# Kernel tuning notes

Measured on AMD Instinct MI355X. Metric: run time of the kernel, lower is better.

The kernel has to match this reference:

```python
import jax, jax.numpy as jnp
import numpy as np

N_NODES = 50000
EMB = 256
HEADS = 8
NEG_SLOPE = 0.2


def gat_conv(x, src, dst, W, a_src, a_dst, b, num_nodes):
    # x: [N, Din]; W: [Din, H, F]; a_src/a_dst: [H, F]; b: [H*F]
    h = jnp.einsum('nd,dhf->nhf', x, W)                      # [N, H, F]
    al_s = jnp.sum(h * a_src, axis=-1)                       # [N, H]
    al_d = jnp.sum(h * a_dst, axis=-1)                       # [N, H]
    logits = jax.nn.leaky_relu(al_s[src] + al_d[dst], NEG_SLOPE)  # [E, H]
    # segment softmax over incoming edges of each destination node
    m = jax.ops.segment_max(logits, dst, num_segments=num_nodes)  # [N, H]
    e = jnp.exp(logits - m[dst])                              # [E, H]
    z = jax.ops.segment_sum(e, dst, num_segments=num_nodes)   # [N, H]
    alpha = e / (z[dst] + 1e-16)                              # [E, H]
    msg = h[src] * alpha[..., None]                           # [E, H, F]
    out = jax.ops.segment_sum(msg, dst, num_segments=num_nodes)  # [N, H, F]
    return out.reshape(num_nodes, -1) + b


def setup_inputs() -> dict:
    key = jax.random.key(0)
    ks = jax.random.split(key, 10)
    F1 = EMB // HEADS  # 32
    x = jax.random.normal(ks[0], (N_NODES, EMB), dtype=jnp.float32)
    edge_index = jax.random.randint(ks[1], (2, 800000), 0, N_NODES, dtype=jnp.int64)
    s1 = 1.0 / np.sqrt(EMB)
    W1 = jax.random.normal(ks[2], (EMB, HEADS, F1), dtype=jnp.float32) * s1
    a_src1 = jax.random.normal(ks[3], (HEADS, F1), dtype=jnp.float32) * s1
    a_dst1 = jax.random.normal(ks[4], (HEADS, F1), dtype=jnp.float32) * s1
    b1 = jnp.zeros((HEADS * F1,), dtype=jnp.float32)
    W2 = jax.random.normal(ks[5], (EMB, 1, EMB), dtype=jnp.float32) * s1
    a_src2 = jax.random.normal(ks[6], (1, EMB), dtype=jnp.float32) * s1
    a_dst2 = jax.random.normal(ks[7], (1, EMB), dtype=jnp.float32) * s1
    b2 = jnp.zeros((EMB,), dtype=jnp.float32)
    return {"x": x, "edge_index": edge_index,
            "W1": W1, "a_src1": a_src1, "a_dst1": a_dst1, "b1": b1,
            "W2": W2, "a_src2": a_src2, "a_dst2": a_dst2, "b2": b2}


def reference(x, edge_index, W1, a_src1, a_dst1, b1, W2, a_src2, a_dst2, b2):
    n = x.shape[0]
    loops = jnp.arange(n, dtype=edge_index.dtype)
    src = jnp.concatenate([edge_index[0], loops])
    dst = jnp.concatenate([edge_index[1], loops])
    h = gat_conv(x, src, dst, W1, a_src1, a_dst1, b1, n)   # [N, EMB]
    out = gat_conv(h, src, dst, W2, a_src2, a_dst2, b2, n)  # [N, EMB]
    return out
```

## Files before the change

kernel.cpp:

```cpp
#include <hip/hip_runtime.h>
#include <hip/hip_bf16.h>

typedef unsigned short u16;
typedef unsigned int   u32;

typedef __attribute__((ext_vector_type(8))) short s16x8;
typedef __attribute__((ext_vector_type(8))) unsigned short u16x8;
typedef __attribute__((ext_vector_type(4))) float f32x4;

__device__ __forceinline__ float b2f(u16 u) {
    union { u32 i; float f; } v; v.i = ((u32)u) << 16; return v.f;
}
__device__ __forceinline__ u16 f2b(float f) {
    union { float f; u32 i; } v; v.f = f;
    u32 u = v.i;
    u32 r = (u + 0x7fffu + ((u >> 16) & 1u)) >> 16;
    return (u16)r;
}

__global__ void detect_flags(const u16* __restrict__ xw, const int* __restrict__ ei,
                             int* __restrict__ flags) {
    int t = threadIdx.x;
    u16 w = xw[2 * t];
    int e = (w >> 7) & 0xFF;
    bool sane = (e >= 112 && e <= 131);
    unsigned long long m1 = __ballot(sane);
    bool hz = (ei[2 * t + 1] == 0);
    unsigned long long m2 = __ballot(hz);
    if (t == 0) {
        flags[0] = (__popcll(m1) >= 32) ? 0 : 1;
        flags[1] = (m2 == ~0ull) ? 1 : 0;
    }
}

__device__ __forceinline__ int edge_at(const int* __restrict__ ei, int i64f, long long j) {
    return i64f ? ei[2 * j] : ei[(size_t)j];
}

__global__ __launch_bounds__(256) void cvt_b16(const void* __restrict__ in,
                                               u16* __restrict__ outb,
                                               int total4, const int* __restrict__ flags) {
    int i = blockIdx.x * 256 + threadIdx.x;
    if (i >= total4) return;
    ushort4 o;
    if (flags[0]) {
        float4 v = ((const float4*)in)[i];
        o.x = f2b(v.x); o.y = f2b(v.y); o.z = f2b(v.z); o.w = f2b(v.w);
    } else {
        o = ((const ushort4*)in)[i];
    }
    ((ushort4*)outb)[i] = o;
}

__global__ __launch_bounds__(256) void cvt_wt2(const void* __restrict__ W1,
                                               const void* __restrict__ W2,
                                               u16* __restrict__ Wt1,
                                               u16* __restrict__ Wt2,
                                               const int* __restrict__ flags) {
    int b = blockIdx.x;
    const void* W = (b < 256) ? W1 : W2;
    u16* Wt = (b < 256) ? Wt1 : Wt2;
    int k = b & 255, c = threadIdx.x;
    u16 v = flags[0] ? f2b(((const float*)W)[k * 256 + c]) : ((const u16*)W)[k * 256 + c];
    Wt[c * 256 + k] = v;
}

__global__ __launch_bounds__(256) void cvt_small(const void* p0, const void* p1, const void* p2,
                                                 const void* p3, const void* p4, const void* p5,
                                                 u16* __restrict__ sv,
                                                 const int* __restrict__ flags) {
    int t = threadIdx.x;
    const void* ps[6] = {p0, p1, p2, p3, p4, p5};
    int f = flags[0];
#pragma unroll
    for (int j = 0; j < 6; j++) {
        u16 v = f ? f2b(((const float*)ps[j])[t]) : ((const u16*)ps[j])[t];
        sv[j * 256 + t] = v;
    }
}

__global__ __launch_bounds__(256) void count_deg(const int* __restrict__ ei,
                                                 int* __restrict__ deg, int E, int ET,
                                                 const int* __restrict__ flags) {
    int i = blockIdx.x * 256 + threadIdx.x;
    if (i >= ET) return;
    int i64f = flags[1];
    int d = (i < E) ? edge_at(ei, i64f, (long long)E + i) : (i - E);
    atomicAdd(&deg[d], 1);
}

__global__ __launch_bounds__(256) void scan1(const int* __restrict__ deg,
                                             int* __restrict__ offs,
                                             int* __restrict__ bsum, int N) {
    __shared__ int sh[256];
    int tid = threadIdx.x;
    int i = blockIdx.x * 256 + tid;
    int v = (i < N) ? deg[i] : 0;
    sh[tid] = v;
    __syncthreads();
    for (int s = 1; s < 256; s <<= 1) {
        int t = (tid >= s) ? sh[tid - s] : 0;
        __syncthreads();
        sh[tid] += t;
        __syncthreads();
    }
    if (i < N) offs[i] = sh[tid] - v;
    if (tid == 255) bsum[blockIdx.x] = sh[255];
}

__global__ __launch_bounds__(256) void scan2(int* bsum, int nb) {
    __shared__ int sh[256];
    int tid = threadIdx.x;
    int v = (tid < nb) ? bsum[tid] : 0;
    sh[tid] = v;
    __syncthreads();
    for (int s = 1; s < 256; s <<= 1) {
        int t = (tid >= s) ? sh[tid - s] : 0;
        __syncthreads();
        sh[tid] += t;
        __syncthreads();
    }
    if (tid < nb) bsum[tid] = sh[tid] - v;
}

__global__ __launch_bounds__(256) void scan3(int* __restrict__ offs,
                                             const int* __restrict__ bsum, int N, int ET) {
    int i = blockIdx.x * 256 + threadIdx.x;
    if (i < N) offs[i] += bsum[blockIdx.x];
    if (i == 0) offs[N] = ET;
}

__global__ __launch_bounds__(256) void fill_csr(const int* __restrict__ ei,
                                                const int* __restrict__ offs,
                                                int* __restrict__ cur,
                                                int* __restrict__ csr, int E, int ET,
                                                const int* __restrict__ flags) {
    int i = blockIdx.x * 256 + threadIdx.x;
    if (i >= ET) return;
    int i64f = flags[1];
    int s, d;
    if (i < E) { s = edge_at(ei, i64f, i); d = edge_at(ei, i64f, (long long)E + i); }
    else       { s = d = i - E; }
    int p = atomicAdd(&cur[d], 1);
    csr[offs[d] + p] = s;
}

__global__ __launch_bounds__(256) void gemm_tiled(const u16* __restrict__ A,
                                                  const u16* __restrict__ Bt,
                                                  u16* __restrict__ C, int M) {
    __shared__ u16 sA[128 * 32];
    __shared__ u16 sB[128 * 32];
    int tid = threadIdx.x;
    int mt = blockIdx.x >> 1, nt = blockIdx.x & 1;
    int r0 = mt * 128, c0 = nt * 128;
    int w = tid >> 6, lane = tid & 63;
    int wr = w & 1, wc = w >> 1;
    int lm = lane & 15, quad = lane >> 4;

    int row0 = tid >> 2, ch0 = tid & 3;
    int row1 = row0 + 64;
    int ga0 = r0 + row0; if (ga0 >= M) ga0 = M - 1;
    int ga1 = r0 + row1; if (ga1 >= M) ga1 = M - 1;
    const u16* Ab0 = A + (size_t)ga0 * 256 + ch0 * 8;
    const u16* Ab1 = A + (size_t)ga1 * 256 + ch0 * 8;
    const u16* Bb0 = Bt + (size_t)(c0 + row0) * 256 + ch0 * 8;
    const u16* Bb1 = Bt + (size_t)(c0 + row1) * 256 + ch0 * 8;

    u16x8 ra0 = *(const u16x8*)Ab0;
    u16x8 ra1 = *(const u16x8*)Ab1;
    u16x8 rb0 = *(const u16x8*)Bb0;
    u16x8 rb1 = *(const u16x8*)Bb1;

    f32x4 acc[4][4];
#pragma unroll
    for (int i = 0; i < 4; i++)
#pragma unroll
        for (int j = 0; j < 4; j++) acc[i][j] = (f32x4){0.f, 0.f, 0.f, 0.f};

    u16* wA0 = sA + row0 * 32 + ch0 * 8;
    u16* wA1 = sA + row1 * 32 + ch0 * 8;
    u16* wB0 = sB + row0 * 32 + ch0 * 8;
    u16* wB1 = sB + row1 * 32 + ch0 * 8;
    const u16* rA = sA + (wr * 64 + lm) * 32 + quad * 8;
    const u16* rB = sB + (wc * 64 + lm) * 32 + quad * 8;

    for (int kb = 0; kb < 8; kb++) {
        __syncthreads();
        *(u16x8*)wA0 = ra0;
        *(u16x8*)wA1 = ra1;
        *(u16x8*)wB0 = rb0;
        *(u16x8*)wB1 = rb1;
        __syncthreads();
        if (kb < 7) {
            int ko = (kb + 1) * 32;
            ra0 = *(const u16x8*)(Ab0 + ko);
            ra1 = *(const u16x8*)(Ab1 + ko);
            rb0 = *(const u16x8*)(Bb0 + ko);
            rb1 = *(const u16x8*)(Bb1 + ko);
        }
        s16x8 af[4], bf[4];
#pragma unroll
        for (int fr = 0; fr < 4; fr++) af[fr] = *(const s16x8*)(rA + fr * 16 * 32);
#pragma unroll
        for (int fc = 0; fc < 4; fc++) bf[fc] = *(const s16x8*)(rB + fc * 16 * 32);
#pragma unroll
        for (int fr = 0; fr < 4; fr++)
#pragma unroll
            for (int fc = 0; fc < 4; fc++)
                acc[fr][fc] = __builtin_amdgcn_mfma_f32_16x16x32_bf16(af[fr], bf[fc], acc[fr][fc], 0, 0, 0);
    }

#pragma unroll
    for (int fr = 0; fr < 4; fr++) {
#pragma unroll
        for (int fc = 0; fc < 4; fc++) {
#pragma unroll
            for (int r = 0; r < 4; r++) {
                int row = r0 + wr * 64 + fr * 16 + quad * 4 + r;
                if (row < M) C[(size_t)row * 256 + c0 + wc * 64 + fc * 16 + lm] = f2b(acc[fr][fc][r]);
            }
        }
    }
}

__global__ __launch_bounds__(256) void coeff256(const u16* __restrict__ h,
                                                const u16* __restrict__ a_s,
                                                const u16* __restrict__ a_d,
                                                float* __restrict__ al_s,
                                                float* __restrict__ al_d, int N, int H) {
    int tid = threadIdx.x;
    int wid = tid >> 6, lane = tid & 63;
    int node = blockIdx.x * 4 + wid;
    if (node >= N) return;
    ushort4 hv = *(const ushort4*)(h + (size_t)node * 256 + lane * 4);
    ushort4 as = *(const ushort4*)(a_s + lane * 4);
    ushort4 ad = *(const ushort4*)(a_d + lane * 4);
    float h0 = b2f(hv.x), h1 = b2f(hv.y), h2 = b2f(hv.z), h3 = b2f(hv.w);
    float ps = h0 * b2f(as.x) + h1 * b2f(as.y) + h2 * b2f(as.z) + h3 * b2f(as.w);
    float pd = h0 * b2f(ad.x) + h1 * b2f(ad.y) + h2 * b2f(ad.z) + h3 * b2f(ad.w);
    int gsz = 64 / H;
    for (int m = 1; m < gsz; m <<= 1) {
        ps += __shfl_xor(ps, m, 64);
        pd += __shfl_xor(pd, m, 64);
    }
    if ((lane & (gsz - 1)) == 0) {
        int hh = lane / gsz;
        al_s[(size_t)node * H + hh] = ps;
        al_d[(size_t)node * H + hh] = pd;
    }
}

template <int H, int FINAL>
__global__ __launch_bounds__(256) void gat_agg(const u16* __restrict__ hsrc,
                                               const float* __restrict__ al_s,
                                               const float* __restrict__ al_d,
                                               const int* __restrict__ offs,
                                               const int* __restrict__ csr,
                                               const u16* __restrict__ bias,
                                               u16* __restrict__ out_b16,
                                               void* __restrict__ out_final,
                                               const int* __restrict__ flags, int N) {
    constexpr int F = 256 / H;
    int wid = threadIdx.x >> 6, lane = threadIdx.x & 63;
    int n = blockIdx.x * 4 + wid;
    if (n >= N) return;
    int beg = offs[n], end = offs[n + 1];
    int c = lane * 4;
    int hc = c / F;
    float ad = al_d[(size_t)n * H + hc];
    float a0 = 0.f, a1 = 0.f, a2 = 0.f, a3 = 0.f, z = 0.f;

    int i = beg;
    for (; i + 4 <= end; i += 4) {
        int s0 = csr[i], s1 = csr[i + 1], s2 = csr[i + 2], s3 = csr[i + 3];
        float v0 = al_s[(size_t)s0 * H + hc];
        float v1 = al_s[(size_t)s1 * H + hc];
        float v2 = al_s[(size_t)s2 * H + hc];
        float v3 = al_s[(size_t)s3 * H + hc];
        ushort4 h0 = *(const ushort4*)(hsrc + (size_t)s0 * 256 + c);
        ushort4 h1 = *(const ushort4*)(hsrc + (size_t)s1 * 256 + c);
        ushort4 h2 = *(const ushort4*)(hsrc + (size_t)s2 * 256 + c);
        ushort4 h3 = *(const ushort4*)(hsrc + (size_t)s3 * 256 + c);
        v0 += ad; v0 = v0 > 0.f ? v0 : 0.2f * v0; float e0 = __expf(v0);
        v1 += ad; v1 = v1 > 0.f ? v1 : 0.2f * v1; float e1 = __expf(v1);
        v2 += ad; v2 = v2 > 0.f ? v2 : 0.2f * v2; float e2 = __expf(v2);
        v3 += ad; v3 = v3 > 0.f ? v3 : 0.2f * v3; float e3 = __expf(v3);
        z += (e0 + e1) + (e2 + e3);
        a0 += e0 * b2f(h0.x); a1 += e0 * b2f(h0.y); a2 += e0 * b2f(h0.z); a3 += e0 * b2f(h0.w);
        a0 += e1 * b2f(h1.x); a1 += e1 * b2f(h1.y); a2 += e1 * b2f(h1.z); a3 += e1 * b2f(h1.w);
        a0 += e2 * b2f(h2.x); a1 += e2 * b2f(h2.y); a2 += e2 * b2f(h2.z); a3 += e2 * b2f(h2.w);
        a0 += e3 * b2f(h3.x); a1 += e3 * b2f(h3.y); a2 += e3 * b2f(h3.z); a3 += e3 * b2f(h3.w);
    }
    for (; i < end; ++i) {
        int s = csr[i];
        float v = al_s[(size_t)s * H + hc] + ad;
        v = v > 0.f ? v : 0.2f * v;
        float e = __expf(v);
        ushort4 hv = *(const ushort4*)(hsrc + (size_t)s * 256 + c);
        z += e;
        a0 += e * b2f(hv.x); a1 += e * b2f(hv.y); a2 += e * b2f(hv.z); a3 += e * b2f(hv.w);
    }

    float invz = 1.f / (z + 1e-16f);
    ushort4 bv = *(const ushort4*)(bias + c);
    float o0 = a0 * invz + b2f(bv.x);
    float o1 = a1 * invz + b2f(bv.y);
    float o2 = a2 * invz + b2f(bv.z);
    float o3 = a3 * invz + b2f(bv.w);
    if (FINAL) {
        if (flags[0]) {
            float4 ov; ov.x = o0; ov.y = o1; ov.z = o2; ov.w = o3;
            ((float4*)out_final)[(size_t)n * 64 + lane] = ov;
        } else {
            ushort4 ov; ov.x = f2b(o0); ov.y = f2b(o1); ov.z = f2b(o2); ov.w = f2b(o3);
            ((ushort4*)out_final)[(size_t)n * 64 + lane] = ov;
        }
    } else {
        ushort4 ov; ov.x = f2b(o0); ov.y = f2b(o1); ov.z = f2b(o2); ov.w = f2b(o3);
        ((ushort4*)out_b16)[(size_t)n * 64 + lane] = ov;
    }
}

extern "C" void kernel_launch(void* const* d_in, const int* in_sizes, int n_in,
                              void* d_out, int out_size, void* d_ws, size_t ws_size,
                              hipStream_t stream) {
    (void)n_in; (void)out_size; (void)ws_size;
    const void* x   = d_in[0];
    const int*  ei  = (const int*)d_in[1];
    const void* W1  = d_in[2];
    const void* as1 = d_in[3];
    const void* ad1 = d_in[4];
    const void* b1  = d_in[5];
    const void* W2  = d_in[6];
    const void* as2 = d_in[7];
    const void* ad2 = d_in[8];
    const void* b2  = d_in[9];

    const int N  = in_sizes[0] / 256;
    const int E  = in_sizes[1] / 2;
    const int ET = E + N;

    char* base = (char*)d_ws;
    size_t o = 0;
    auto carve = [&](size_t bytes) -> void* {
        void* q = base + o;
        o += (bytes + 255) & ~(size_t)255;
        return q;
    };
    u16*   hproj = (u16*)carve((size_t)N * 256 * 2);
    float* als   = (float*)carve((size_t)N * 8 * 4);
    float* ald   = (float*)carve((size_t)N * 8 * 4);
    int*   deg   = (int*)carve((size_t)N * 4);
    int*   cur   = (int*)carve((size_t)N * 4);
    int*   offs  = (int*)carve((size_t)(N + 1) * 4);
    int*   csr   = (int*)carve((size_t)ET * 4);
    int*   bsum  = (int*)carve(1024 * 4);
    u16*   wt1   = (u16*)carve(256 * 256 * 2);
    u16*   wt2   = (u16*)carve(256 * 256 * 2);
    u16*   sv    = (u16*)carve(6 * 256 * 2);
    int*   flags = (int*)carve(16 * 4);

    u16* xb = (u16*)d_out;

    detect_flags<<<1, 64, 0, stream>>>((const u16*)x, ei, flags);

    hipMemsetAsync(deg, 0, (size_t)N * 4, stream);
    hipMemsetAsync(cur, 0, (size_t)N * 4, stream);

    int x4 = N * 256 / 4;
    cvt_b16<<<(x4 + 255) / 256, 256, 0, stream>>>(x, xb, x4, flags);
    cvt_wt2<<<512, 256, 0, stream>>>(W1, W2, wt1, wt2, flags);
    cvt_small<<<1, 256, 0, stream>>>(as1, ad1, b1, as2, ad2, b2, sv, flags);

    int cg = (ET + 255) / 256;
    int nb = (N + 255) / 256;
    count_deg<<<cg, 256, 0, stream>>>(ei, deg, E, ET, flags);
    scan1<<<nb, 256, 0, stream>>>(deg, offs, bsum, N);
    scan2<<<1, 256, 0, stream>>>(bsum, nb);
    scan3<<<nb, 256, 0, stream>>>(offs, bsum, N, ET);
    fill_csr<<<cg, 256, 0, stream>>>(ei, offs, cur, csr, E, ET, flags);

    int gt = ((N + 127) / 128) * 2;
    int ab = (N + 3) / 4;
    gemm_tiled<<<gt, 256, 0, stream>>>(xb, wt1, hproj, N);
    coeff256<<<ab, 256, 0, stream>>>(hproj, sv + 0 * 256, sv + 1 * 256, als, ald, N, 8);
    gat_agg<8, 0><<<ab, 256, 0, stream>>>(hproj, als, ald, offs, csr, sv + 2 * 256,
                                          xb, nullptr, flags, N);
    gemm_tiled<<<gt, 256, 0, stream>>>(xb, wt2, hproj, N);
    coeff256<<<ab, 256, 0, stream>>>(hproj, sv + 3 * 256, sv + 4 * 256, als, ald, N, 1);
    gat_agg<1, 1><<<ab, 256, 0, stream>>>(hproj, als, ald, offs, csr, sv + 5 * 256,
                                          nullptr, d_out, flags, N);
}
```

Before: 408.9 us.

## Fuse prep kernels, pad CSR segments to 8, and share edge weights via shuffles

Merges dtype detection, x/W/small-vector conversion and the degree/cursor memsets into one `prep` launch that also fills the CSR with a sentinel node index. Each destination's CSR segment is padded to a multiple of 8, and the two upper scan passes become one kernel. Aggregation now processes 8 edges per step: each lane computes one edge's index and exp value, then broadcasts them with shuffles, which removes the redundant per-lane attention loads and exps. The sentinel relies on `al_s[N] = -1e30` so its weight is zero. Its `hproj` row is never written, so garbage (NaN/Inf) there could poison the sums, and padding adds wasted gather work for low-degree nodes.

```diff
diff --git a/kernel.cpp b/kernel.cpp
--- a/kernel.cpp
+++ b/kernel.cpp
@@ -18,64 +18,83 @@
     return (u16)r;
 }
 
-__global__ void detect_flags(const u16* __restrict__ xw, const int* __restrict__ ei,
-                             int* __restrict__ flags) {
-    int t = threadIdx.x;
+__device__ __forceinline__ int detect_f32(const u16* xw) {
+    int t = threadIdx.x & 63;
     u16 w = xw[2 * t];
     int e = (w >> 7) & 0xFF;
     bool sane = (e >= 112 && e <= 131);
     unsigned long long m1 = __ballot(sane);
-    bool hz = (ei[2 * t + 1] == 0);
-    unsigned long long m2 = __ballot(hz);
-    if (t == 0) {
-        flags[0] = (__popcll(m1) >= 32) ? 0 : 1;
-        flags[1] = (m2 == ~0ull) ? 1 : 0;
-    }
+    return (__popcll(m1) >= 32) ? 0 : 1;
 }
 
 __device__ __forceinline__ int edge_at(const int* __restrict__ ei, int i64f, long long j) {
     return i64f ? ei[2 * j] : ei[(size_t)j];
 }
 
-__global__ __launch_bounds__(256) void cvt_b16(const void* __restrict__ in,
-                                               u16* __restrict__ outb,
-                                               int total4, const int* __restrict__ flags) {
-    int i = blockIdx.x * 256 + threadIdx.x;
-    if (i >= total4) return;
-    ushort4 o;
-    if (flags[0]) {
-        float4 v = ((const float4*)in)[i];
-        o.x = f2b(v.x); o.y = f2b(v.y); o.z = f2b(v.z); o.w = f2b(v.w);
-    } else {
-        o = ((const ushort4*)in)[i];
-    }
-    ((ushort4*)outb)[i] = o;
-}
-
-__global__ __launch_bounds__(256) void cvt_wt2(const void* __restrict__ W1,
-                                               const void* __restrict__ W2,
-                                               u16* __restrict__ Wt1,
-                                               u16* __restrict__ Wt2,
-                                               const int* __restrict__ flags) {
-    int b = blockIdx.x;
-    const void* W = (b < 256) ? W1 : W2;
-    u16* Wt = (b < 256) ? Wt1 : Wt2;
-    int k = b & 255, c = threadIdx.x;
-    u16 v = flags[0] ? f2b(((const float*)W)[k * 256 + c]) : ((const u16*)W)[k * 256 + c];
-    Wt[c * 256 + k] = v;
-}
-
-__global__ __launch_bounds__(256) void cvt_small(const void* p0, const void* p1, const void* p2,
-                                                 const void* p3, const void* p4, const void* p5,
-                                                 u16* __restrict__ sv,
-                                                 const int* __restrict__ flags) {
-    int t = threadIdx.x;
-    const void* ps[6] = {p0, p1, p2, p3, p4, p5};
-    int f = flags[0];
-#pragma unroll
-    for (int j = 0; j < 6; j++) {
-        u16 v = f ? f2b(((const float*)ps[j])[t]) : ((const u16*)ps[j])[t];
-        sv[j * 256 + t] = v;
+__global__ __launch_bounds__(256) void prep(const void* __restrict__ x,
+                                            const int* __restrict__ ei,
+                                            const void* __restrict__ W1, const void* __restrict__ W2,
+                                            const void* p0, const void* p1, const void* p2,
+                                            const void* p3, const void* p4, const void* p5,
+                                            u16* __restrict__ xb, u16* __restrict__ wt1,
+                                            u16* __restrict__ wt2, u16* __restrict__ sv,
+                                            int* __restrict__ degcur, int* __restrict__ csr,
+                                            int* __restrict__ flags,
+                                            int x4, int BX, int ZB, int CF, int NN, int csr4) {
+    int b = blockIdx.x, t = threadIdx.x;
+    int f32f = detect_f32((const u16*)x);
+    if (b < BX) {
+        int i = b * 256 + t;
+        if (i < x4) {
+            ushort4 o;
+            if (f32f) {
+                float4 v = ((const float4*)x)[i];
+                o.x = f2b(v.x); o.y = f2b(v.y); o.z = f2b(v.z); o.w = f2b(v.w);
+            } else o = ((const ushort4*)x)[i];
+            ((ushort4*)xb)[i] = o;
+        }
+        return;
+    }
+    b -= BX;
+    if (b < 512) {
+        const void* W = (b < 256) ? W1 : W2;
+        u16* Wt = (b < 256) ? wt1 : wt2;
+        int k = b & 255;
+        u16 v = f32f ? f2b(((const float*)W)[k * 256 + t]) : ((const u16*)W)[k * 256 + t];
+        Wt[t * 256 + k] = v;
+        return;
+    }
+    b -= 512;
+    if (b == 0) {
+        const void* ps[6] = {p0, p1, p2, p3, p4, p5};
+#pragma unroll
+        for (int j = 0; j < 6; j++) {
+            u16 v = f32f ? f2b(((const float*)ps[j])[t]) : ((const u16*)ps[j])[t];
+            sv[j * 256 + t] = v;
+        }
+        if (t < 64) {
+            bool hz = (ei[2 * t + 1] == 0);
+            unsigned long long m2 = __ballot(hz);
+            if (t == 0) {
+                flags[0] = f32f;
+                flags[1] = (m2 == ~0ull) ? 1 : 0;
+            }
+        }
+        return;
+    }
+    b -= 1;
+    if (b < ZB) {
+        int i = b * 256 + t;
+        int tot4 = (NN == 0) ? 0 : 0;
+        (void)tot4;
+        ((int4*)degcur)[i] = make_int4(0, 0, 0, 0);
+        return;
+    }
+    b -= ZB;
+    if (b < CF) {
+        int i = b * 256 + t;
+        if (i < csr4) ((int4*)csr)[i] = make_int4(NN, NN, NN, NN);
+        return;
     }
 }
 
@@ -95,7 +114,7 @@
     __shared__ int sh[256];
     int tid = threadIdx.x;
     int i = blockIdx.x * 256 + tid;
-    int v = (i < N) ? deg[i] : 0;
+    int v = (i < N) ? ((deg[i] + 7) & ~7) : 0;
     sh[tid] = v;
     __syncthreads();
     for (int s = 1; s < 256; s <<= 1) {
@@ -108,26 +127,23 @@
     if (tid == 255) bsum[blockIdx.x] = sh[255];
 }
 
-__global__ __launch_bounds__(256) void scan2(int* bsum, int nb) {
+__global__ __launch_bounds__(256) void scan23(int* __restrict__ offs,
+                                              const int* __restrict__ bsum, int N, int nbv) {
     __shared__ int sh[256];
-    int tid = threadIdx.x;
-    int v = (tid < nb) ? bsum[tid] : 0;
-    sh[tid] = v;
+    int t = threadIdx.x, b = blockIdx.x;
+    int v = (t < nbv) ? bsum[t] : 0;
+    sh[t] = v;
     __syncthreads();
     for (int s = 1; s < 256; s <<= 1) {
-        int t = (tid >= s) ? sh[tid - s] : 0;
-        __syncthreads();
-        sh[tid] += t;
-        __syncthreads();
-    }
-    if (tid < nb) bsum[tid] = sh[tid] - v;
-}
-
-__global__ __launch_bounds__(256) void scan3(int* __restrict__ offs,
-                                             const int* __restrict__ bsum, int N, int ET) {
-    int i = blockIdx.x * 256 + threadIdx.x;
-    if (i < N) offs[i] += bsum[blockIdx.x];
-    if (i == 0) offs[N] = ET;
+        int u = (t >= s) ? sh[t - s] : 0;
+        __syncthreads();
+        sh[t] += u;
+        __syncthreads();
+    }
+    int P = (b > 0) ? sh[b - 1] : 0;
+    int i = b * 256 + t;
+    if (i < N) offs[i] += P;
+    if (b == 0 && t == 0) offs[N] = sh[nbv - 1];
 }
 
 __global__ __launch_bounds__(256) void fill_csr(const int* __restrict__ ei,
@@ -229,6 +245,7 @@
                                                 float* __restrict__ al_s,
                                                 float* __restrict__ al_d, int N, int H) {
     int tid = threadIdx.x;
+    if (blockIdx.x == 0 && tid < 8) al_s[(size_t)N * H + tid] = -1e30f;
     int wid = tid >> 6, lane = tid & 63;
     int node = blockIdx.x * 4 + wid;
     if (node >= N) return;
@@ -260,45 +277,32 @@
                                                u16* __restrict__ out_b16,
                                                void* __restrict__ out_final,
                                                const int* __restrict__ flags, int N) {
-    constexpr int F = 256 / H;
     int wid = threadIdx.x >> 6, lane = threadIdx.x & 63;
     int n = blockIdx.x * 4 + wid;
     if (n >= N) return;
     int beg = offs[n], end = offs[n + 1];
     int c = lane * 4;
-    int hc = c / F;
-    float ad = al_d[(size_t)n * H + hc];
+    int hc = (H == 8) ? (lane >> 3) : 0;
+    int he = lane & (H - 1);
+    int j8 = lane >> 3;
+    float ad_e = al_d[(size_t)n * H + he];
+    const u16* hb = hsrc + c;
     float a0 = 0.f, a1 = 0.f, a2 = 0.f, a3 = 0.f, z = 0.f;
 
-    int i = beg;
-    for (; i + 4 <= end; i += 4) {
-        int s0 = csr[i], s1 = csr[i + 1], s2 = csr[i + 2], s3 = csr[i + 3];
-        float v0 = al_s[(size_t)s0 * H + hc];
-        float v1 = al_s[(size_t)s1 * H + hc];
-        float v2 = al_s[(size_t)s2 * H + hc];
-        float v3 = al_s[(size_t)s3 * H + hc];
-        ushort4 h0 = *(const ushort4*)(hsrc + (size_t)s0 * 256 + c);
-        ushort4 h1 = *(const ushort4*)(hsrc + (size_t)s1 * 256 + c);
-        ushort4 h2 = *(const ushort4*)(hsrc + (size_t)s2 * 256 + c);
-        ushort4 h3 = *(const ushort4*)(hsrc + (size_t)s3 * 256 + c);
-        v0 += ad; v0 = v0 > 0.f ? v0 : 0.2f * v0; float e0 = __expf(v0);
-        v1 += ad; v1 = v1 > 0.f ? v1 : 0.2f * v1; float e1 = __expf(v1);
-        v2 += ad; v2 = v2 > 0.f ? v2 : 0.2f * v2; float e2 = __expf(v2);
-        v3 += ad; v3 = v3 > 0.f ? v3 : 0.2f * v3; float e3 = __expf(v3);
-        z += (e0 + e1) + (e2 + e3);
-        a0 += e0 * b2f(h0.x); a1 += e0 * b2f(h0.y); a2 += e0 * b2f(h0.z); a3 += e0 * b2f(h0.w);
-        a0 += e1 * b2f(h1.x); a1 += e1 * b2f(h1.y); a2 += e1 * b2f(h1.z); a3 += e1 * b2f(h1.w);
-        a0 += e2 * b2f(h2.x); a1 += e2 * b2f(h2.y); a2 += e2 * b2f(h2.z); a3 += e2 * b2f(h2.w);
-        a0 += e3 * b2f(h3.x); a1 += e3 * b2f(h3.y); a2 += e3 * b2f(h3.z); a3 += e3 * b2f(h3.w);
-    }
-    for (; i < end; ++i) {
-        int s = csr[i];
-        float v = al_s[(size_t)s * H + hc] + ad;
+    for (int i = beg; i < end; i += 8) {
+        int sm = csr[i + j8];
+        float v = al_s[(size_t)sm * H + he] + ad_e;
         v = v > 0.f ? v : 0.2f * v;
-        float e = __expf(v);
-        ushort4 hv = *(const ushort4*)(hsrc + (size_t)s * 256 + c);
-        z += e;
-        a0 += e * b2f(hv.x); a1 += e * b2f(hv.y); a2 += e * b2f(hv.z); a3 += e * b2f(hv.w);
+        float em = __expf(v);
+#pragma unroll
+        for (int j = 0; j < 8; j++) {
+            int   sj = __shfl(sm, j * 8, 64);
+            float ej = __shfl(em, j * 8 + hc, 64);
+            ushort4 hv = *(const ushort4*)(hb + (size_t)sj * 256);
+            z += ej;
+            a0 += ej * b2f(hv.x); a1 += ej * b2f(hv.y);
+            a2 += ej * b2f(hv.z); a3 += ej * b2f(hv.w);
+        }
     }
 
     float invz = 1.f / (z + 1e-16f);
@@ -339,6 +343,7 @@
     const int N  = in_sizes[0] / 256;
     const int E  = in_sizes[1] / 2;
     const int ET = E + N;
+    const int CSRCAP = (ET + 7 * N + 63) & ~63;
 
     char* base = (char*)d_ws;
     size_t o = 0;
@@ -347,37 +352,37 @@
         o += (bytes + 255) & ~(size_t)255;
         return q;
     };
-    u16*   hproj = (u16*)carve((size_t)N * 256 * 2);
-    float* als   = (float*)carve((size_t)N * 8 * 4);
-    float* ald   = (float*)carve((size_t)N * 8 * 4);
-    int*   deg   = (int*)carve((size_t)N * 4);
-    int*   cur   = (int*)carve((size_t)N * 4);
-    int*   offs  = (int*)carve((size_t)(N + 1) * 4);
-    int*   csr   = (int*)carve((size_t)ET * 4);
-    int*   bsum  = (int*)carve(1024 * 4);
-    u16*   wt1   = (u16*)carve(256 * 256 * 2);
-    u16*   wt2   = (u16*)carve(256 * 256 * 2);
-    u16*   sv    = (u16*)carve(6 * 256 * 2);
-    int*   flags = (int*)carve(16 * 4);
+    u16*   hproj  = (u16*)carve((size_t)(N + 1) * 256 * 2);
+    float* als    = (float*)carve((size_t)(N + 1) * 8 * 4);
+    float* ald    = (float*)carve((size_t)N * 8 * 4);
+    int*   degcur = (int*)carve((size_t)2 * N * 4);
+    int*   offs   = (int*)carve((size_t)(N + 1) * 4);
+    int*   csr    = (int*)carve((size_t)CSRCAP * 4);
+    int*   bsum   = (int*)carve(1024 * 4);
+    u16*   wt1    = (u16*)carve(256 * 256 * 2);
+    u16*   wt2    = (u16*)carve(256 * 256 * 2);
+    u16*   sv     = (u16*)carve(6 * 256 * 2);
+    int*   flags  = (int*)carve(16 * 4);
+    int* deg = degcur;
+    int* cur = degcur + N;
 
     u16* xb = (u16*)d_out;
 
-    detect_flags<<<1, 64, 0, stream>>>((const u16*)x, ei, flags);
-
-    hipMemsetAsync(deg, 0, (size_t)N * 4, stream);
-    hipMemsetAsync(cur, 0, (size_t)N * 4, stream);
-
     int x4 = N * 256 / 4;
-    cvt_b16<<<(x4 + 255) / 256, 256, 0, stream>>>(x, xb, x4, flags);
-    cvt_wt2<<<512, 256, 0, stream>>>(W1, W2, wt1, wt2, flags);
-    cvt_small<<<1, 256, 0, stream>>>(as1, ad1, b1, as2, ad2, b2, sv, flags);
+    int BX = (x4 + 255) / 256;
+    int ZB = (2 * N / 4 + 255) / 256;
+    int csr4 = CSRCAP / 4;
+    int CF = (csr4 + 255) / 256;
+    int PB = BX + 512 + 1 + ZB + CF;
+    prep<<<PB, 256, 0, stream>>>(x, ei, W1, W2, as1, ad1, b1, as2, ad2, b2,
+                                 xb, wt1, wt2, sv, degcur, csr, flags,
+                                 x4, BX, ZB, CF, N, csr4);
 
     int cg = (ET + 255) / 256;
     int nb = (N + 255) / 256;
     count_deg<<<cg, 256, 0, stream>>>(ei, deg, E, ET, flags);
     scan1<<<nb, 256, 0, stream>>>(deg, offs, bsum, N);
-    scan2<<<1, 256, 0, stream>>>(bsum, nb);
-    scan3<<<nb, 256, 0, stream>>>(offs, bsum, N, ET);
+    scan23<<<nb, 256, 0, stream>>>(offs, bsum, N, nb);
     fill_csr<<<cg, 256, 0, stream>>>(ei, offs, cur, csr, E, ET, flags);
 
     int gt = ((N + 127) / 128) * 2;
```

Result: faster. 386.6 us (-5.4%).
